# Performance work log

Hardware: AMD Instinct MI355X
Metric: run time of the kernel (lower is better)

Reference implementation:

```python
import jax, jax.numpy as jnp
import numpy as np

N_NODES = 100000
N_EDGES = 625000
D = 128


def setup_inputs() -> dict:
    key = jax.random.key(0)
    ks = jax.random.split(key, 6)
    x = jax.random.normal(ks[0], (N_NODES, D), dtype=jnp.float32)
    src = jax.random.randint(ks[1], (N_EDGES,), 0, N_NODES, dtype=jnp.int32)
    dst = jnp.sort(jax.random.randint(ks[2], (N_EDGES,), 0, N_NODES, dtype=jnp.int32))
    edge_w = jax.random.uniform(ks[3], (N_EDGES,), dtype=jnp.float32)
    # linear layer params (fan-in scaled)
    W = jax.random.normal(ks[4], (D, D), dtype=jnp.float32) / np.sqrt(D)
    b = jnp.zeros((D,), dtype=jnp.float32)
    # highway gate params (glorot-uniform-ish range as in source)
    init_range = np.sqrt(2.0 / (D + D)).astype(np.float32)
    kernel_gate = jax.random.uniform(ks[5], (D, D), dtype=jnp.float32,
                                     minval=-init_range, maxval=init_range)
    bias_gate = jnp.zeros((D,), dtype=jnp.float32)
    return {"x": x, "src": src, "dst": dst, "edge_w": edge_w,
            "W": W, "b": b, "kernel_gate": kernel_gate, "bias_gate": bias_gate}


def reference(x, src, dst, edge_w, W, b, kernel_gate, bias_gate):
    # hidden = Linear(x); dropout is identity in eval mode
    hidden = x @ W.T + b                                  # [N, D]
    # support = spmm(adj, hidden): gather src rows, weight, scatter-add to dst
    msgs = edge_w[:, None] * hidden[src]                  # [E, D]
    support = jax.ops.segment_sum(msgs, dst, num_segments=x.shape[0])
    support = jax.nn.relu(support)                        # act
    # highway gate
    gate = jax.nn.sigmoid(x @ kernel_gate + bias_gate)    # [N, D]
    out = gate * support + (1.0 - gate) * x
    return out
```

## Files before the change

kernel.cpp:

```cpp
#include <hip/hip_runtime.h>

#define DD 128

typedef __attribute__((ext_vector_type(8))) short bf16x8;
typedef __attribute__((ext_vector_type(4))) float f32x4;

__device__ __forceinline__ unsigned int cvt_pk_bf16(float lo, float hi) {
  unsigned int r;
  asm("v_cvt_pk_bf16_f32 %0, %1, %2" : "=v"(r) : "v"(lo), "v"(hi));
  return r;
}
__device__ __forceinline__ float bf_lo(unsigned int v) { return __uint_as_float(v << 16); }
__device__ __forceinline__ float bf_hi(unsigned int v) { return __uint_as_float(v & 0xFFFF0000u); }

__global__ void prep_kernel(const float* __restrict__ x, const int* __restrict__ dst,
                            const float* __restrict__ W, const float* __restrict__ KG,
                            unsigned short* __restrict__ xb, int* __restrict__ row_start,
                            unsigned short* __restrict__ B, int N, int E) {
  int i = blockIdx.x * 256 + threadIdx.x;
  int NC = N * (DD / 4);
  if (i < NC) {
    float4 v = ((const float4*)x)[i];
    uint2 q = {cvt_pk_bf16(v.x, v.y), cvt_pk_bf16(v.z, v.w)};
    ((uint2*)xb)[i] = q;
  } else if (i < NC + E + 1) {
    int e = i - NC;
    if (e == 0) {
      int d0 = dst[0];
      for (int n = 0; n <= d0; ++n) row_start[n] = 0;
    } else if (e == E) {
      for (int n = dst[E - 1] + 1; n <= N; ++n) row_start[n] = E;
    } else {
      int d = dst[e], dp = dst[e - 1];
      for (int n = dp + 1; n <= d; ++n) row_start[n] = e;
    }
  } else if (i < NC + E + 1 + 2 * DD * DD) {
    int e2 = i - (NC + E + 1);
    int j = e2 >> 7, k = e2 & 127;
    float v = (j < DD) ? W[j * DD + k] : KG[k * DD + (j - DD)];
    B[e2] = (unsigned short)cvt_pk_bf16(v, v);
  }
}

__global__ __launch_bounds__(256, 8) void scatter_agg(
    const unsigned short* __restrict__ xb, const int* __restrict__ src,
    const float* __restrict__ ew, const int* __restrict__ row_start,
    unsigned short* __restrict__ aggb, float* __restrict__ sumw) {
  int w = threadIdx.x >> 6;
  int lane = threadIdx.x & 63;
  int n = blockIdx.x * 4 + w;
  int b = __builtin_amdgcn_readfirstlane(row_start[n]);
  int e = __builtin_amdgcn_readfirstlane(row_start[n + 1]);
  const unsigned int* x32 = (const unsigned int*)xb;

  float a0x = 0.f, a0y = 0.f, a1x = 0.f, a1y = 0.f;
  float a2x = 0.f, a2y = 0.f, a3x = 0.f, a3y = 0.f;
  float ws_ = 0.f;
  int i = b;
  for (; i + 4 <= e; i += 4) {
    int s0 = src[i], s1 = src[i + 1], s2 = src[i + 2], s3 = src[i + 3];
    float w0 = ew[i], w1 = ew[i + 1], w2 = ew[i + 2], w3 = ew[i + 3];
    unsigned int v0 = x32[(size_t)s0 * 64 + lane];
    unsigned int v1 = x32[(size_t)s1 * 64 + lane];
    unsigned int v2 = x32[(size_t)s2 * 64 + lane];
    unsigned int v3 = x32[(size_t)s3 * 64 + lane];
    a0x += w0 * bf_lo(v0); a0y += w0 * bf_hi(v0);
    a1x += w1 * bf_lo(v1); a1y += w1 * bf_hi(v1);
    a2x += w2 * bf_lo(v2); a2y += w2 * bf_hi(v2);
    a3x += w3 * bf_lo(v3); a3y += w3 * bf_hi(v3);
    ws_ += w0 + w1 + w2 + w3;
  }
  for (; i < e; ++i) {
    int s = src[i];
    float wt = ew[i];
    unsigned int v = x32[(size_t)s * 64 + lane];
    a0x += wt * bf_lo(v); a0y += wt * bf_hi(v);
    ws_ += wt;
  }
  float ax = a0x + a1x + a2x + a3x;
  float ay = a0y + a1y + a2y + a3y;
  ((unsigned int*)aggb)[(size_t)n * 64 + lane] = cvt_pk_bf16(ax, ay);
  if (lane == 0) sumw[n] = ws_;
}

__global__ __launch_bounds__(256, 2) void fused_gemm(
    const unsigned short* __restrict__ xb, const unsigned short* __restrict__ aggb,
    const unsigned short* __restrict__ B, const float* __restrict__ sumw,
    const float* __restrict__ bias, const float* __restrict__ bg,
    float* __restrict__ out, int N) {
  __shared__ char smem[32 * 1024];
  unsigned short* sX = (unsigned short*)smem;
  unsigned short* sA = (unsigned short*)(smem + 16384);
  int t = threadIdx.x;
  int wid = t >> 6, lane = t & 63;
  int lr = lane & 15, lk2 = lane >> 4;
  int jw = wid * 32;
  int M0 = blockIdx.x * 64;

  bf16x8 wS[4][2], wG[4][2];
#pragma unroll
  for (int kc = 0; kc < 4; ++kc)
#pragma unroll
    for (int m = 0; m < 2; ++m) {
      int j = jw + m * 16 + lr;
      wS[kc][m] = *(const bf16x8*)(B + (size_t)j * DD + kc * 32 + lk2 * 8);
      wG[kc][m] = *(const bf16x8*)(B + (size_t)(DD + j) * DD + kc * 32 + lk2 * 8);
    }
  float b4[2][4], bg4[2][4];
#pragma unroll
  for (int m = 0; m < 2; ++m) {
    *(float4*)b4[m]  = *(const float4*)&bias[jw + m * 16 + lk2 * 4];
    *(float4*)bg4[m] = *(const float4*)&bg[jw + m * 16 + lk2 * 4];
  }

#pragma unroll
  for (int i = 0; i < 4; ++i) {
    int idx = i * 256 + t;
    int r = idx >> 4, c = idx & 15;
    uint4 vx, va;
    if (M0 + r < N) {
      vx = ((const uint4*)(xb + (size_t)(M0 + r) * DD))[c];
      va = ((const uint4*)(aggb + (size_t)(M0 + r) * DD))[c];
    } else {
      vx = make_uint4(0, 0, 0, 0);
      va = make_uint4(0, 0, 0, 0);
    }
    int off = (r * 256 + c * 16) ^ ((r & 7) << 4);
    *(uint4*)((char*)sX + off) = vx;
    *(uint4*)((char*)sA + off) = va;
  }
  __syncthreads();

  f32x4 accS[2][4], accG[2][4];
#pragma unroll
  for (int m = 0; m < 2; ++m)
#pragma unroll
    for (int nr = 0; nr < 4; ++nr) {
      accS[m][nr] = (f32x4){0.f, 0.f, 0.f, 0.f};
      accG[m][nr] = (f32x4){0.f, 0.f, 0.f, 0.f};
    }

#pragma unroll
  for (int kc = 0; kc < 4; ++kc) {
    int kb = (kc * 32 + lk2 * 8) * 2;
    bf16x8 af[4], xf[4];
#pragma unroll
    for (int nr = 0; nr < 4; ++nr) {
      int r = nr * 16 + lr;
      int off = (r * 256 + kb) ^ ((r & 7) << 4);
      af[nr] = *(const bf16x8*)((const char*)sA + off);
      xf[nr] = *(const bf16x8*)((const char*)sX + off);
    }
#pragma unroll
    for (int m = 0; m < 2; ++m)
#pragma unroll
      for (int nr = 0; nr < 4; ++nr) {
        accS[m][nr] = __builtin_amdgcn_mfma_f32_16x16x32_bf16(wS[kc][m], af[nr], accS[m][nr], 0, 0, 0);
        accG[m][nr] = __builtin_amdgcn_mfma_f32_16x16x32_bf16(wG[kc][m], xf[nr], accG[m][nr], 0, 0, 0);
      }
  }

#pragma unroll
  for (int m = 0; m < 2; ++m) {
    int j0 = jw + m * 16 + lk2 * 4;
#pragma unroll
    for (int nr = 0; nr < 4; ++nr) {
      int node = M0 + nr * 16 + lr;
      if (node < N) {
        float sw = sumw[node];
        int r = nr * 16 + lr;
        uint2 qx = *(const uint2*)((const char*)sX + ((r * 256 + j0 * 2) ^ ((r & 7) << 4)));
        float xr[4] = {bf_lo(qx.x), bf_hi(qx.x), bf_lo(qx.y), bf_hi(qx.y)};
        f32x4 vs = accS[m][nr], vg = accG[m][nr];
        float4 o;
        float* op = &o.x;
#pragma unroll
        for (int reg = 0; reg < 4; ++reg) {
          float s = fmaxf(vs[reg] + sw * b4[m][reg], 0.f);
          float g = 1.0f / (1.0f + __expf(-(vg[reg] + bg4[m][reg])));
          op[reg] = g * s + (1.0f - g) * xr[reg];
        }
        *(float4*)&out[(size_t)node * DD + j0] = o;
      }
    }
  }
}

extern "C" void kernel_launch(void* const* d_in, const int* in_sizes, int n_in,
                              void* d_out, int out_size, void* d_ws, size_t ws_size,
                              hipStream_t stream) {
  const float* x   = (const float*)d_in[0];
  const int*   src = (const int*)d_in[1];
  const int*   dst = (const int*)d_in[2];
  const float* ew  = (const float*)d_in[3];
  const float* W   = (const float*)d_in[4];
  const float* b   = (const float*)d_in[5];
  const float* KG  = (const float*)d_in[6];
  const float* bg  = (const float*)d_in[7];
  float* out = (float*)d_out;

  int N = in_sizes[0] / DD;
  int E = in_sizes[1];

  unsigned short* xbuf = (unsigned short*)d_ws;
  unsigned short* aggb = xbuf + (size_t)N * DD;
  unsigned short* B    = aggb + (size_t)N * DD;
  float* sumw = (float*)(B + 2 * DD * DD);
  int* row_start = (int*)(sumw + N);

  int totalPrep = N * (DD / 4) + (E + 1) + 2 * DD * DD;
  prep_kernel<<<(totalPrep + 255) / 256, 256, 0, stream>>>(x, dst, W, KG, xbuf, row_start, B, N, E);
  scatter_agg<<<N / 4, 256, 0, stream>>>(xbuf, src, ew, row_start, aggb, sumw);
  fused_gemm<<<(N + 63) / 64, 256, 0, stream>>>(xbuf, aggb, B, sumw, b, bg, out, N);
}
```

Measured before the change: 83.71 us.

## Process four nodes per wavefront in scatter aggregation with 16-byte gathers

The aggregation kernel now gives each 16-lane quarter of a wavefront its own destination node. Each lane gathers a 16-byte (8 bf16) chunk of the source row instead of 4 bytes. This cuts the number of gather instructions and raises bytes per load, and it fits the low average degree of about six edges per node. In exchange, quarters whose nodes have fewer edges idle while the wave loops until the longest row finishes, and they do clamped dummy loads meanwhile.

```diff
diff --git a/kernel.cpp b/kernel.cpp
--- a/kernel.cpp
+++ b/kernel.cpp
@@ -45,42 +45,51 @@
 __global__ __launch_bounds__(256, 8) void scatter_agg(
     const unsigned short* __restrict__ xb, const int* __restrict__ src,
     const float* __restrict__ ew, const int* __restrict__ row_start,
-    unsigned short* __restrict__ aggb, float* __restrict__ sumw) {
-  int w = threadIdx.x >> 6;
-  int lane = threadIdx.x & 63;
-  int n = blockIdx.x * 4 + w;
-  int b = __builtin_amdgcn_readfirstlane(row_start[n]);
-  int e = __builtin_amdgcn_readfirstlane(row_start[n + 1]);
-  const unsigned int* x32 = (const unsigned int*)xb;
-
-  float a0x = 0.f, a0y = 0.f, a1x = 0.f, a1y = 0.f;
-  float a2x = 0.f, a2y = 0.f, a3x = 0.f, a3y = 0.f;
-  float ws_ = 0.f;
-  int i = b;
-  for (; i + 4 <= e; i += 4) {
-    int s0 = src[i], s1 = src[i + 1], s2 = src[i + 2], s3 = src[i + 3];
-    float w0 = ew[i], w1 = ew[i + 1], w2 = ew[i + 2], w3 = ew[i + 3];
-    unsigned int v0 = x32[(size_t)s0 * 64 + lane];
-    unsigned int v1 = x32[(size_t)s1 * 64 + lane];
-    unsigned int v2 = x32[(size_t)s2 * 64 + lane];
-    unsigned int v3 = x32[(size_t)s3 * 64 + lane];
-    a0x += w0 * bf_lo(v0); a0y += w0 * bf_hi(v0);
-    a1x += w1 * bf_lo(v1); a1y += w1 * bf_hi(v1);
-    a2x += w2 * bf_lo(v2); a2y += w2 * bf_hi(v2);
-    a3x += w3 * bf_lo(v3); a3y += w3 * bf_hi(v3);
-    ws_ += w0 + w1 + w2 + w3;
-  }
-  for (; i < e; ++i) {
-    int s = src[i];
-    float wt = ew[i];
-    unsigned int v = x32[(size_t)s * 64 + lane];
-    a0x += wt * bf_lo(v); a0y += wt * bf_hi(v);
-    ws_ += wt;
-  }
-  float ax = a0x + a1x + a2x + a3x;
-  float ay = a0y + a1y + a2y + a3y;
-  ((unsigned int*)aggb)[(size_t)n * 64 + lane] = cvt_pk_bf16(ax, ay);
-  if (lane == 0) sumw[n] = ws_;
+    unsigned short* __restrict__ aggb, float* __restrict__ sumw, int N, int E) {
+  int t = threadIdx.x;
+  int wid = t >> 6, lane = t & 63;
+  int q = lane >> 4, lr = lane & 15;
+  int n = blockIdx.x * 16 + wid * 4 + q;
+  bool valid = (n < N);
+  int b = valid ? row_start[n] : 0;
+  int cnt = valid ? (row_start[n + 1] - b) : 0;
+  const uint4* x16 = (const uint4*)xb;
+
+  float a[8];
+#pragma unroll
+  for (int k = 0; k < 8; ++k) a[k] = 0.f;
+  float wsum = 0.f;
+  int clampj = cnt > 0 ? cnt - 1 : 0;
+
+  int i = 0;
+  while (__any(i < cnt)) {
+#pragma unroll
+    for (int u = 0; u < 4; ++u) {
+      int ii = i + u;
+      int jj = ii < clampj ? ii : clampj;
+      int j = b + jj;
+      if (j > E - 1) j = E - 1;
+      float wt = (ii < cnt) ? ew[j] : 0.f;
+      int s = src[j];
+      uint4 v = x16[(size_t)s * 16 + lr];
+      wsum += wt;
+      a[0] += wt * bf_lo(v.x); a[1] += wt * bf_hi(v.x);
+      a[2] += wt * bf_lo(v.y); a[3] += wt * bf_hi(v.y);
+      a[4] += wt * bf_lo(v.z); a[5] += wt * bf_hi(v.z);
+      a[6] += wt * bf_lo(v.w); a[7] += wt * bf_hi(v.w);
+    }
+    i += 4;
+  }
+
+  if (valid) {
+    uint4 o;
+    o.x = cvt_pk_bf16(a[0], a[1]);
+    o.y = cvt_pk_bf16(a[2], a[3]);
+    o.z = cvt_pk_bf16(a[4], a[5]);
+    o.w = cvt_pk_bf16(a[6], a[7]);
+    ((uint4*)aggb)[(size_t)n * 16 + lr] = o;
+    if (lr == 0) sumw[n] = wsum;
+  }
 }
 
 __global__ __launch_bounds__(256, 2) void fused_gemm(
@@ -210,6 +219,6 @@
 
   int totalPrep = N * (DD / 4) + (E + 1) + 2 * DD * DD;
   prep_kernel<<<(totalPrep + 255) / 256, 256, 0, stream>>>(x, dst, W, KG, xbuf, row_start, B, N, E);
-  scatter_agg<<<N / 4, 256, 0, stream>>>(xbuf, src, ew, row_start, aggb, sumw);
+  scatter_agg<<<(N + 15) / 16, 256, 0, stream>>>(xbuf, src, ew, row_start, aggb, sumw, N, E);
   fused_gemm<<<(N + 63) / 64, 256, 0, stream>>>(xbuf, aggb, B, sumw, b, bg, out, N);
 }
```

Measured after the change: 81.73 us. 1.02x faster.
